# Kernel optimization log

Hardware: AMD Instinct MI355X
Metric: run time of the kernel (lower is better)

## Reference

```python
import jax, jax.numpy as jnp
import numpy as np

D, H, W = 8, 64, 64  # image_shape
EPS = 1e-6
LOG_2PI = float(np.log(2.0 * np.pi))


def _pixel_positions():
    z = jnp.arange(D, dtype=jnp.float32) - (D - 1) / 2.0
    y = jnp.arange(H, dtype=jnp.float32) - (H - 1) / 2.0
    x = jnp.arange(W, dtype=jnp.float32) - (W - 1) / 2.0
    zg, yg, xg = jnp.meshgrid(z, y, x, indexing='ij')  # [D,H,W]
    return jnp.stack([xg, yg, zg], axis=-1).reshape(-1, 3)  # [N,3], order (x,y,z)


def setup_inputs() -> dict:
    key = jax.random.key(0)
    ks = jax.random.split(key, 5)
    return {
        'representation': jax.random.normal(ks[0], (1024, 256), dtype=jnp.float32),
        'mean_W': jax.random.normal(ks[1], (3, 256), dtype=jnp.float32) * 0.05,
        'mean_b': jax.random.normal(ks[2], (3,), dtype=jnp.float32) * 0.05,
        'scale_W': jax.random.normal(ks[3], (6, 256), dtype=jnp.float32) * 0.05,
        'scale_b': jax.random.normal(ks[4], (6,), dtype=jnp.float32) * 0.05,
    }


def reference(representation, mean_W, mean_b, scale_W, scale_b):
    # tiny projections
    means = representation @ mean_W.T + mean_b          # [B,3]
    raw = representation @ scale_W.T + scale_b          # [B,6]
    s = jax.nn.softplus(raw) + EPS                      # softplus in forward
    # FillScaleTriL: vec -> lower-tri (row-major: (0,0),(1,0),(1,1),(2,0),(2,1),(2,2)),
    # then softplus applied again to the diagonal only.
    L00 = jax.nn.softplus(s[:, 0])
    L10 = s[:, 1]
    L11 = jax.nn.softplus(s[:, 2])
    L20 = s[:, 3]
    L21 = s[:, 4]
    L22 = jax.nn.softplus(s[:, 5])

    pix = _pixel_positions()                            # [N,3]
    diff = pix[None, :, :] - means[:, None, :]          # [B,N,3]
    # hardcoded 3x3 forward-substitution: y = L^{-1} diff
    y0 = diff[..., 0] / L00[:, None]
    y1 = (diff[..., 1] - L10[:, None] * y0) / L11[:, None]
    y2 = (diff[..., 2] - L20[:, None] * y0 - L21[:, None] * y1) / L22[:, None]
    maha = y0 * y0 + y1 * y1 + y2 * y2                  # [B,N]
    log_det = jnp.log(L00) + jnp.log(L11) + jnp.log(L22)  # [B]
    log_probs = -0.5 * maha - log_det[:, None] - 1.5 * LOG_2PI  # [B,N]

    log_probs_stable = log_probs - jnp.max(log_probs, axis=1, keepdims=True)
    profile = jnp.exp(log_probs_stable)
    profile = profile / (jnp.sum(profile, axis=1, keepdims=True) + 1e-10)
    return profile
```

## Files before the change

### kernel.cpp

```cpp
#include <hip/hip_runtime.h>
#include <math.h>

#define NG    1024
#define KD    256
#define NPIX  32768
#define BLOCK 512

#define LN2PI_15  2.7568155996140185f
#define LOG2E     1.4426950408889634f
#define SQH_L2E   0.8493218f

__device__ __forceinline__ float softplus_f(float x) {
    return fmaxf(x, 0.0f) + log1pf(expf(-fabsf(x)));
}

__device__ __forceinline__ float exp2_fast(float x) {
#if __has_builtin(__builtin_amdgcn_exp2f)
    return __builtin_amdgcn_exp2f(x);
#else
    float r; asm("v_exp_f32 %0, %1" : "=v"(r) : "v"(x)); return r;
#endif
}

__global__ __launch_bounds__(BLOCK, 8)
void mvn_profile_kernel(const float* __restrict__ rep,
                        const float* __restrict__ mean_W,
                        const float* __restrict__ mean_b,
                        const float* __restrict__ scale_W,
                        const float* __restrict__ scale_b,
                        float* __restrict__ out)
{
    const int g = blockIdx.x;
    const int t = threadIdx.x;

    __shared__ float s_part[9][4];
    __shared__ float s_par[10];
    __shared__ float s_red[8];

    if (t < KD) {
        float r = rep[g * KD + t];
        float acc9[9];
        #pragma unroll
        for (int k = 0; k < 3; ++k) acc9[k]     = r * mean_W[k * KD + t];
        #pragma unroll
        for (int k = 0; k < 6; ++k) acc9[3 + k] = r * scale_W[k * KD + t];
        #pragma unroll
        for (int k = 0; k < 9; ++k) {
            float v = acc9[k];
            #pragma unroll
            for (int off = 32; off >= 1; off >>= 1)
                v += __shfl_xor(v, off, 64);
            if ((t & 63) == 0) s_part[k][t >> 6] = v;
        }
    }
    __syncthreads();
    if (t == 0) {
        float dsum[9];
        #pragma unroll
        for (int k = 0; k < 9; ++k)
            dsum[k] = (s_part[k][0] + s_part[k][1]) + (s_part[k][2] + s_part[k][3]);
        float mx = dsum[0] + mean_b[0];
        float my = dsum[1] + mean_b[1];
        float mz = dsum[2] + mean_b[2];
        float s0 = softplus_f(dsum[3] + scale_b[0]) + 1e-6f;
        float s1 = softplus_f(dsum[4] + scale_b[1]) + 1e-6f;
        float s2 = softplus_f(dsum[5] + scale_b[2]) + 1e-6f;
        float s3 = softplus_f(dsum[6] + scale_b[3]) + 1e-6f;
        float s4 = softplus_f(dsum[7] + scale_b[4]) + 1e-6f;
        float s5 = softplus_f(dsum[8] + scale_b[5]) + 1e-6f;
        float L00 = softplus_f(s0);
        float L11 = softplus_f(s2);
        float L22 = softplus_f(s5);
        s_par[0] = mx; s_par[1] = my; s_par[2] = mz;
        s_par[3] = 1.0f / L00;
        s_par[4] = s1;
        s_par[5] = 1.0f / L11;
        s_par[6] = s3;
        s_par[7] = s4;
        s_par[8] = SQH_L2E / L22;
        s_par[9] = -LOG2E * (logf(L00) + logf(L11) + logf(L22) + LN2PI_15);
    }
    __syncthreads();
    const float mx   = s_par[0], my  = s_par[1], mz  = s_par[2];
    const float r00  = s_par[3], L10 = s_par[4], r11 = s_par[5];
    const float L20  = s_par[6], L21 = s_par[7], r22s = s_par[8];
    const float c0   = s_par[9];
    const float mzc  = -3.5f - mz;

    const float xb = (float)(4 * (t & 15)) - 31.5f - mx;
    const float f0 = (float)(t >> 4);
    float urs[8], base[8];
    #pragma unroll
    for (int k = 0; k < 4; ++k) {
        float y0  = (xb + (float)k) * r00;
        float y0s = y0 * SQH_L2E;
        float b0  = fmaf(-y0s, y0s, c0);
        float dzk = fmaf(-L20, y0, mzc);
        float dyk = fmaf(-L10, y0, -31.5f - my);
        #pragma unroll
        for (int f = 0; f < 2; ++f) {
            float py  = f0 + (float)(32 * f);
            float y1  = (py + dyk) * r11;
            float y1s = y1 * SQH_L2E;
            base[k*2+f] = fmaf(-y1s, y1s, b0);
            urs [k*2+f] = fmaf(-L21, y1, dzk) * r22s;
        }
    }

    float acc0 = 0.f, acc1 = 0.f, acc2 = 0.f, acc3 = 0.f;
    #pragma unroll
    for (int i = 0; i < 16; ++i) {
        const int   fs = i & 1;
        const float fz = (float)(i >> 1);
        {
            float y2s = fmaf(fz, r22s, urs[0*2+fs]);
            acc0 += exp2_fast(fmaf(-y2s, y2s, base[0*2+fs]));
        }
        {
            float y2s = fmaf(fz, r22s, urs[1*2+fs]);
            acc1 += exp2_fast(fmaf(-y2s, y2s, base[1*2+fs]));
        }
        {
            float y2s = fmaf(fz, r22s, urs[2*2+fs]);
            acc2 += exp2_fast(fmaf(-y2s, y2s, base[2*2+fs]));
        }
        {
            float y2s = fmaf(fz, r22s, urs[3*2+fs]);
            acc3 += exp2_fast(fmaf(-y2s, y2s, base[3*2+fs]));
        }
    }
    float lsum = (acc0 + acc1) + (acc2 + acc3);
    #pragma unroll
    for (int off = 32; off >= 1; off >>= 1)
        lsum += __shfl_xor(lsum, off, 64);
    if ((t & 63) == 0) s_red[t >> 6] = lsum;
    __syncthreads();
    float S = 0.0f;
    #pragma unroll
    for (int k = 0; k < 8; ++k) S += s_red[k];

    const float lS = log2f(S + 1e-10f);
    #pragma unroll
    for (int k = 0; k < 8; ++k) base[k] -= lS;

    float4* op4 = (float4*)(out + (size_t)g * NPIX) + t;
    #pragma unroll
    for (int i = 0; i < 16; ++i) {
        const int   fs = i & 1;
        const float fz = (float)(i >> 1);
        float4 o;
        { float y2s = fmaf(fz, r22s, urs[0*2+fs]); o.x = exp2_fast(fmaf(-y2s, y2s, base[0*2+fs])); }
        { float y2s = fmaf(fz, r22s, urs[1*2+fs]); o.y = exp2_fast(fmaf(-y2s, y2s, base[1*2+fs])); }
        { float y2s = fmaf(fz, r22s, urs[2*2+fs]); o.z = exp2_fast(fmaf(-y2s, y2s, base[2*2+fs])); }
        { float y2s = fmaf(fz, r22s, urs[3*2+fs]); o.w = exp2_fast(fmaf(-y2s, y2s, base[3*2+fs])); }
        op4[i * 512] = o;
    }
}

extern "C" void kernel_launch(void* const* d_in, const int* in_sizes, int n_in,
                              void* d_out, int out_size, void* d_ws, size_t ws_size,
                              hipStream_t stream) {
    const float* rep     = (const float*)d_in[0];
    const float* mean_W  = (const float*)d_in[1];
    const float* mean_b  = (const float*)d_in[2];
    const float* scale_W = (const float*)d_in[3];
    const float* scale_b = (const float*)d_in[4];
    float* out = (float*)d_out;

    hipLaunchKernelGGL(mvn_profile_kernel, dim3(NG), dim3(BLOCK), 0, stream,
                       rep, mean_W, mean_b, scale_W, scale_b, out);
}
```

Baseline: 169.7 us.

## Split fused kernel into reduce pass and write pass over half-volumes

Splits the single fused kernel into two launches. The first computes the per-Gaussian parameters and the normalisation sum, storing them in the workspace. The second launches twice as many blocks, each writing half of one Gaussian's output volume. The aim is to separate the exp-heavy reduction from the store-bound write phase and give the write phase more parallelism, at the cost of an extra launch and recomputing the per-thread setup terms.

After: 156.0 us. -8.1%, faster.

```diff
diff --git a/kernel.cpp b/kernel.cpp
--- a/kernel.cpp
+++ b/kernel.cpp
@@ -1,10 +1,12 @@
 #include <hip/hip_runtime.h>
 #include <math.h>
 
-#define NG    1024
-#define KD    256
-#define NPIX  32768
-#define BLOCK 512
+#define NG     1024
+#define KD     256
+#define NPIX   32768
+#define B1     512
+#define B2     512
+#define PSTR   12
 
 #define LN2PI_15  2.7568155996140185f
 #define LOG2E     1.4426950408889634f
@@ -22,13 +24,14 @@
 #endif
 }
 
-__global__ __launch_bounds__(BLOCK, 8)
-void mvn_profile_kernel(const float* __restrict__ rep,
-                        const float* __restrict__ mean_W,
-                        const float* __restrict__ mean_b,
-                        const float* __restrict__ scale_W,
-                        const float* __restrict__ scale_b,
-                        float* __restrict__ out)
+
+__global__ __launch_bounds__(B1)
+void mvn_reduce_kernel(const float* __restrict__ rep,
+                       const float* __restrict__ mean_W,
+                       const float* __restrict__ mean_b,
+                       const float* __restrict__ scale_W,
+                       const float* __restrict__ scale_b,
+                       float* __restrict__ ws)
 {
     const int g = blockIdx.x;
     const int t = threadIdx.x;
@@ -71,21 +74,23 @@
         float L00 = softplus_f(s0);
         float L11 = softplus_f(s2);
         float L22 = softplus_f(s5);
-        s_par[0] = mx; s_par[1] = my; s_par[2] = mz;
-        s_par[3] = 1.0f / L00;
-        s_par[4] = s1;
-        s_par[5] = 1.0f / L11;
-        s_par[6] = s3;
-        s_par[7] = s4;
-        s_par[8] = SQH_L2E / L22;
-        s_par[9] = -LOG2E * (logf(L00) + logf(L11) + logf(L22) + LN2PI_15);
+        float par[10];
+        par[0] = mx; par[1] = my; par[2] = mz;
+        par[3] = 1.0f / L00;
+        par[4] = s1;
+        par[5] = 1.0f / L11;
+        par[6] = s3;
+        par[7] = s4;
+        par[8] = SQH_L2E / L22;
+        par[9] = -LOG2E * (logf(L00) + logf(L11) + logf(L22) + LN2PI_15);
+        #pragma unroll
+        for (int k = 0; k < 10; ++k) { s_par[k] = par[k]; ws[g * PSTR + k] = par[k]; }
     }
     __syncthreads();
-    const float mx   = s_par[0], my  = s_par[1], mz  = s_par[2];
-    const float r00  = s_par[3], L10 = s_par[4], r11 = s_par[5];
-    const float L20  = s_par[6], L21 = s_par[7], r22s = s_par[8];
-    const float c0   = s_par[9];
-    const float mzc  = -3.5f - mz;
+    const float mx  = s_par[0], my  = s_par[1], mz  = s_par[2];
+    const float r00 = s_par[3], L10 = s_par[4], r11 = s_par[5];
+    const float L20 = s_par[6], L21 = s_par[7], r22s = s_par[8];
+    const float c0  = s_par[9];
 
     const float xb = (float)(4 * (t & 15)) - 31.5f - mx;
     const float f0 = (float)(t >> 4);
@@ -95,7 +100,7 @@
         float y0  = (xb + (float)k) * r00;
         float y0s = y0 * SQH_L2E;
         float b0  = fmaf(-y0s, y0s, c0);
-        float dzk = fmaf(-L20, y0, mzc);
+        float dzk = fmaf(-L20, y0, -3.5f - mz);
         float dyk = fmaf(-L10, y0, -31.5f - my);
         #pragma unroll
         for (int f = 0; f < 2; ++f) {
@@ -112,22 +117,10 @@
     for (int i = 0; i < 16; ++i) {
         const int   fs = i & 1;
         const float fz = (float)(i >> 1);
-        {
-            float y2s = fmaf(fz, r22s, urs[0*2+fs]);
-            acc0 += exp2_fast(fmaf(-y2s, y2s, base[0*2+fs]));
-        }
-        {
-            float y2s = fmaf(fz, r22s, urs[1*2+fs]);
-            acc1 += exp2_fast(fmaf(-y2s, y2s, base[1*2+fs]));
-        }
-        {
-            float y2s = fmaf(fz, r22s, urs[2*2+fs]);
-            acc2 += exp2_fast(fmaf(-y2s, y2s, base[2*2+fs]));
-        }
-        {
-            float y2s = fmaf(fz, r22s, urs[3*2+fs]);
-            acc3 += exp2_fast(fmaf(-y2s, y2s, base[3*2+fs]));
-        }
+        { float y2s = fmaf(fz, r22s, urs[0+fs]); acc0 += exp2_fast(fmaf(-y2s, y2s, base[0+fs])); }
+        { float y2s = fmaf(fz, r22s, urs[2+fs]); acc1 += exp2_fast(fmaf(-y2s, y2s, base[2+fs])); }
+        { float y2s = fmaf(fz, r22s, urs[4+fs]); acc2 += exp2_fast(fmaf(-y2s, y2s, base[4+fs])); }
+        { float y2s = fmaf(fz, r22s, urs[6+fs]); acc3 += exp2_fast(fmaf(-y2s, y2s, base[6+fs])); }
     }
     float lsum = (acc0 + acc1) + (acc2 + acc3);
     #pragma unroll
@@ -135,24 +128,58 @@
         lsum += __shfl_xor(lsum, off, 64);
     if ((t & 63) == 0) s_red[t >> 6] = lsum;
     __syncthreads();
-    float S = 0.0f;
-    #pragma unroll
-    for (int k = 0; k < 8; ++k) S += s_red[k];
-
-    const float lS = log2f(S + 1e-10f);
-    #pragma unroll
-    for (int k = 0; k < 8; ++k) base[k] -= lS;
-
-    float4* op4 = (float4*)(out + (size_t)g * NPIX) + t;
-    #pragma unroll
-    for (int i = 0; i < 16; ++i) {
+    if (t == 0) {
+        float S = 0.0f;
+        #pragma unroll
+        for (int k = 0; k < 8; ++k) S += s_red[k];
+        ws[g * PSTR + 10] = S;
+    }
+}
+
+__global__ __launch_bounds__(B2)
+void mvn_write_kernel(const float* __restrict__ ws, float* __restrict__ out)
+{
+    const int b    = blockIdx.x;
+    const int g    = b >> 1;
+    const int half = b & 1;
+    const int t    = threadIdx.x;
+
+    const float* P = ws + g * PSTR;
+    const float mx  = P[0], my  = P[1], mz  = P[2];
+    const float r00 = P[3], L10 = P[4], r11 = P[5];
+    const float L20 = P[6], L21 = P[7], r22s = P[8];
+    const float c0n = P[9] - log2f(P[10] + 1e-10f);
+
+    const float xb = (float)(4 * (t & 15)) - 31.5f - mx;
+    const float f0 = (float)(t >> 4);
+    float urs[8], base[8];
+    #pragma unroll
+    for (int k = 0; k < 4; ++k) {
+        float y0  = (xb + (float)k) * r00;
+        float y0s = y0 * SQH_L2E;
+        float b0  = fmaf(-y0s, y0s, c0n);
+        float dzk = fmaf(-L20, y0, -3.5f - mz);
+        float dyk = fmaf(-L10, y0, -31.5f - my);
+        #pragma unroll
+        for (int f = 0; f < 2; ++f) {
+            float py  = f0 + (float)(32 * f);
+            float y1  = (py + dyk) * r11;
+            float y1s = y1 * SQH_L2E;
+            base[k*2+f] = fmaf(-y1s, y1s, b0);
+            urs [k*2+f] = fmaf(-L21, y1, dzk) * r22s;
+        }
+    }
+
+    float4* op4 = (float4*)(out + (size_t)g * NPIX) + half * 4096 + t;
+    #pragma unroll
+    for (int i = 0; i < 8; ++i) {
         const int   fs = i & 1;
-        const float fz = (float)(i >> 1);
+        const float fz = (float)(4 * half + (i >> 1));
         float4 o;
-        { float y2s = fmaf(fz, r22s, urs[0*2+fs]); o.x = exp2_fast(fmaf(-y2s, y2s, base[0*2+fs])); }
-        { float y2s = fmaf(fz, r22s, urs[1*2+fs]); o.y = exp2_fast(fmaf(-y2s, y2s, base[1*2+fs])); }
-        { float y2s = fmaf(fz, r22s, urs[2*2+fs]); o.z = exp2_fast(fmaf(-y2s, y2s, base[2*2+fs])); }
-        { float y2s = fmaf(fz, r22s, urs[3*2+fs]); o.w = exp2_fast(fmaf(-y2s, y2s, base[3*2+fs])); }
+        { float y2s = fmaf(fz, r22s, urs[0+fs]); o.x = exp2_fast(fmaf(-y2s, y2s, base[0+fs])); }
+        { float y2s = fmaf(fz, r22s, urs[2+fs]); o.y = exp2_fast(fmaf(-y2s, y2s, base[2+fs])); }
+        { float y2s = fmaf(fz, r22s, urs[4+fs]); o.z = exp2_fast(fmaf(-y2s, y2s, base[4+fs])); }
+        { float y2s = fmaf(fz, r22s, urs[6+fs]); o.w = exp2_fast(fmaf(-y2s, y2s, base[6+fs])); }
         op4[i * 512] = o;
     }
 }
@@ -166,7 +193,10 @@
     const float* scale_W = (const float*)d_in[3];
     const float* scale_b = (const float*)d_in[4];
     float* out = (float*)d_out;
-
-    hipLaunchKernelGGL(mvn_profile_kernel, dim3(NG), dim3(BLOCK), 0, stream,
-                       rep, mean_W, mean_b, scale_W, scale_b, out);
-}
+    float* ws  = (float*)d_ws;
+
+    hipLaunchKernelGGL(mvn_reduce_kernel, dim3(NG), dim3(B1), 0, stream,
+                       rep, mean_W, mean_b, scale_W, scale_b, ws);
+    hipLaunchKernelGGL(mvn_write_kernel, dim3(2 * NG), dim3(B2), 0, stream,
+                       ws, out);
+}
```
